# Kernel optimization log

Hardware: AMD Instinct MI355X
Metric: run time of the kernel (lower is better)

## Reference

```python
import jax, jax.numpy as jnp
import numpy as np

# Static problem dims (all graphs equal-sized so adaptive pool = uniform bins)
B = 64          # graphs
N = 2048        # nodes per graph
E = 16          # node_emb_dim
H_OUT, W_OUT = 32, 4   # AdaptiveAvgPool2d output -> pooled_dim = 128
COND = 64       # cond_emb_dim
HID = 512       # mlp_h_dim
BN_EPS = 1e-5


def _lin_init(key, out_d, in_d):
    kw, kb = jax.random.split(key)
    lim = 1.0 / np.sqrt(in_d)
    W = jax.random.uniform(kw, (out_d, in_d), jnp.float32, -lim, lim)
    b = jax.random.uniform(kb, (out_d,), jnp.float32, -lim, lim)
    return W, b


def setup_inputs() -> dict:
    key = jax.random.key(0)
    ks = jax.random.split(key, 6)
    Ntot = B * N
    x = jax.random.normal(ks[0], (Ntot, E), jnp.float32)
    batch = jnp.repeat(jnp.arange(B, dtype=jnp.int32), N)  # sorted segment ids
    cond = jax.random.normal(ks[1], (Ntot, COND), jnp.float32)
    mlp_in = COND + H_OUT * W_OUT  # 192
    W1, b1 = _lin_init(ks[2], HID, mlp_in)
    W2, b2 = _lin_init(ks[3], HID, HID)
    W3, b3 = _lin_init(ks[4], 3, HID)
    g1 = jnp.ones((HID,), jnp.float32); be1 = jnp.zeros((HID,), jnp.float32)
    g2 = jnp.ones((HID,), jnp.float32); be2 = jnp.zeros((HID,), jnp.float32)
    return {"x": x, "batch": batch, "conditioner_z_ref": cond,
            "W1": W1, "b1": b1, "g1": g1, "be1": be1,
            "W2": W2, "b2": b2, "g2": g2, "be2": be2,
            "W3": W3, "b3": b3}


def _bn_gelu(h, g, be):
    # BatchNorm1d in training mode: biased batch stats over the node axis
    m = h.mean(axis=0)
    v = h.var(axis=0)
    h = g * (h - m) * jax.lax.rsqrt(v + BN_EPS) + be
    return jax.nn.gelu(h, approximate=False)


def reference(x, batch, conditioner_z_ref, W1, b1, g1, be1, W2, b2, g2, be2, W3, b3):
    # Per-graph adaptive avg pool: since N % H_OUT == 0 and E % W_OUT == 0,
    # AdaptiveAvgPool2d is exactly mean over uniform (N/H_OUT, E/W_OUT) bins.
    xb = x.reshape(B, H_OUT, N // H_OUT, W_OUT, E // W_OUT)
    batch_pooled = xb.mean(axis=(2, 4)).reshape(B, H_OUT * W_OUT)  # [B, 128]
    pooled_per_node = batch_pooled[batch]                           # gather to [Ntot, 128]
    h = jnp.concatenate([conditioner_z_ref, pooled_per_node], axis=1)  # [Ntot, 192]
    h = _bn_gelu(h @ W1.T + b1, g1, be1)
    h = _bn_gelu(h @ W2.T + b2, g2, be2)
    return h @ W3.T + b3  # [Ntot, 3] predicted coords
```

## Files before the change

### kernel.cpp

```cpp
#include <hip/hip_runtime.h>
#include <hip/hip_bf16.h>
#include <math.h>
#include <stdint.h>

#define B_GRAPHS 64
#define N_NODES  2048
#define E_DIM    16
#define M_TOT    (B_GRAPHS * N_NODES)
#define K_COND   64
#define MLP_IN   192
#define HID      512
#define POOLD    128
#define BN_EPS   1e-5f

typedef __attribute__((ext_vector_type(8))) short bfrag8;
typedef __attribute__((ext_vector_type(4))) float facc4;

__device__ __forceinline__ unsigned short f2b(float f) {
    unsigned int x = __builtin_bit_cast(unsigned int, f);
    unsigned int r = x + 0x7fffu + ((x >> 16) & 1u);
    return (unsigned short)(r >> 16);
}
__device__ __forceinline__ float b2f(unsigned short u) {
    unsigned int x = ((unsigned int)u) << 16;
    return __builtin_bit_cast(float, x);
}

__device__ __forceinline__ float gelu_fast(float y) {
    float x  = y * 0.70710678118654752440f;
    float ax = fabsf(x);
    float t  = __builtin_amdgcn_rcpf(fmaf(0.3275911f, ax, 1.0f));
    float p  = fmaf(1.061405429f, t, -1.453152027f);
    p = fmaf(p, t, 1.421413741f);
    p = fmaf(p, t, -0.284496736f);
    p = fmaf(p, t, 0.254829592f);
    p = p * t;
    float e = __expf(-x * x);
    float erfax = fmaf(-p, e, 1.0f);
    float erfx  = copysignf(erfax, x);
    return 0.5f * y * (1.0f + erfx);
}

__global__ __launch_bounds__(512) void prep_kernel(const float* __restrict__ x,
                                                   const float* __restrict__ W1,
                                                   const float* __restrict__ b1,
                                                   float* __restrict__ gbias) {
    __shared__ float pl[POOLD];
    int g = blockIdx.x, t = threadIdx.x;
    if (t < 128) {
        int h = t >> 2, w = t & 3;
        const float* base = x + (size_t)g * N_NODES * E_DIM + (size_t)h * 64 * E_DIM + w * 4;
        float s = 0.f;
        #pragma unroll 4
        for (int r = 0; r < 64; ++r) {
            float4 v = *reinterpret_cast<const float4*>(base + (size_t)r * E_DIM);
            s += v.x + v.y + v.z + v.w;
        }
        pl[h * 4 + w] = s * (1.0f / 256.0f);
    }
    __syncthreads();
    const float* wr_ = W1 + (size_t)t * MLP_IN + K_COND;
    float s = b1[t];
    #pragma unroll 4
    for (int k = 0; k < POOLD; ++k) s = fmaf(pl[k], wr_[k], s);
    gbias[g * HID + t] = s;
}

__global__ __launch_bounds__(256) void cvt_kernel(const float* __restrict__ s,
                                                  unsigned short* __restrict__ d) {
    size_t i = ((size_t)blockIdx.x * 256 + threadIdx.x) * 8;
    float4 v0 = *reinterpret_cast<const float4*>(s + i);
    float4 v1 = *reinterpret_cast<const float4*>(s + i + 4);
    unsigned short t[8] = {f2b(v0.x), f2b(v0.y), f2b(v0.z), f2b(v0.w),
                           f2b(v1.x), f2b(v1.y), f2b(v1.z), f2b(v1.w)};
    *reinterpret_cast<bfrag8*>(d + i) = *reinterpret_cast<bfrag8*>(t);
}

__device__ __forceinline__ bfrag8 load_f32x8_as_bf16(const float* p) {
    float4 v0 = *reinterpret_cast<const float4*>(p);
    float4 v1 = *reinterpret_cast<const float4*>(p + 4);
    unsigned short t[8] = {f2b(v0.x), f2b(v0.y), f2b(v0.z), f2b(v0.w),
                           f2b(v1.x), f2b(v1.y), f2b(v1.z), f2b(v1.w)};
    return *reinterpret_cast<bfrag8*>(t);
}

__global__ __launch_bounds__(512, 1) void gemm1_kernel(const float* __restrict__ A,
                                                       const float* __restrict__ W,
                                                       const float* __restrict__ gbias,
                                                       float* __restrict__ sums,
                                                       unsigned short* __restrict__ C) {
    __shared__ unsigned short As[128 * 64];
    __shared__ float sArr[HID], qArr[HID];
    const int t = threadIdx.x;
    const int r0 = blockIdx.x * 128;
    const int g = r0 >> 11;
    const int l = t & 63, w = t >> 6;
    const int wr = w >> 2, wc = w & 3;
    const int ln = l & 15, kg = l >> 4;
    sArr[t] = 0.f; qArr[t] = 0.f;

    {
        const int cg = t & 7, rb = t >> 3;
        #pragma unroll
        for (int i = 0; i < 2; ++i) {
            int row = rb + i * 64;
            bfrag8 vv = load_f32x8_as_bf16(A + (size_t)(r0 + row) * K_COND + cg * 8);
            int dg = row * 8 + (cg ^ (row & 7));
            *reinterpret_cast<bfrag8*>(&As[dg * 8]) = vv;
        }
    }
    bfrag8 bf0[8], bf1[8];
    #pragma unroll
    for (int b = 0; b < 8; ++b) {
        int RB = wc * 128 + b * 16 + ln;
        bf0[b] = load_f32x8_as_bf16(W + (size_t)RB * MLP_IN + kg * 8);
        bf1[b] = load_f32x8_as_bf16(W + (size_t)RB * MLP_IN + 32 + kg * 8);
    }
    __syncthreads();

    facc4 acc[4][8];
    const facc4 z = {0.f, 0.f, 0.f, 0.f};
    #pragma unroll
    for (int a = 0; a < 4; ++a)
        #pragma unroll
        for (int b = 0; b < 8; ++b) acc[a][b] = z;

    #pragma unroll
    for (int s = 0; s < 2; ++s) {
        bfrag8 af[4];
        #pragma unroll
        for (int a = 0; a < 4; ++a) {
            int RA = wr * 64 + a * 16 + ln;
            af[a] = *reinterpret_cast<const bfrag8*>(&As[(RA * 8 + ((s * 4 + kg) ^ (RA & 7))) * 8]);
        }
        #pragma unroll
        for (int a = 0; a < 4; ++a)
            #pragma unroll
            for (int b = 0; b < 8; ++b)
                acc[a][b] = __builtin_amdgcn_mfma_f32_16x16x32_bf16(
                    af[a], s == 0 ? bf0[b] : bf1[b], acc[a][b], 0, 0, 0);
    }

    const float* gb = gbias + (size_t)g * HID;
    float gbv[8];
    #pragma unroll
    for (int b = 0; b < 8; ++b) gbv[b] = gb[wc * 128 + b * 16 + ln];
    float cs[8], cq[8];
    #pragma unroll
    for (int b = 0; b < 8; ++b) { cs[b] = 0.f; cq[b] = 0.f; }
    #pragma unroll
    for (int a = 0; a < 4; ++a) {
        #pragma unroll
        for (int i = 0; i < 4; ++i) {
            size_t rbase = (size_t)(r0 + wr * 64 + a * 16 + kg * 4 + i) * HID + wc * 128 + ln;
            #pragma unroll
            for (int b = 0; b < 8; ++b) {
                float v = acc[a][b][i] + gbv[b];
                C[rbase + b * 16] = f2b(v);
                cs[b] += v; cq[b] = fmaf(v, v, cq[b]);
            }
        }
    }
    #pragma unroll
    for (int b = 0; b < 8; ++b) {
        cs[b] += __shfl_xor(cs[b], 16, 64); cq[b] += __shfl_xor(cq[b], 16, 64);
        cs[b] += __shfl_xor(cs[b], 32, 64); cq[b] += __shfl_xor(cq[b], 32, 64);
    }
    if (kg == 0) {
        #pragma unroll
        for (int b = 0; b < 8; ++b) {
            int cl = wc * 128 + b * 16 + ln;
            atomicAdd(&sArr[cl], cs[b]); atomicAdd(&qArr[cl], cq[b]);
        }
    }
    __syncthreads();
    atomicAdd(&sums[t], sArr[t]);
    atomicAdd(&sums[HID + t], qArr[t]);
}

__global__ __launch_bounds__(512, 1) void gemm2_kernel(const unsigned short* __restrict__ A,
                                                       const unsigned short* __restrict__ Bm,
                                                       const float* __restrict__ sums1,
                                                       const float* __restrict__ g1,
                                                       const float* __restrict__ be1,
                                                       const float* __restrict__ bias,
                                                       float* __restrict__ sums,
                                                       unsigned short* __restrict__ C) {
    __shared__ unsigned short As[128 * 512];
    __shared__ float sArr[HID], qArr[HID];
    const int t = threadIdx.x;
    const int r0 = blockIdx.x * 128;
    const int l = t & 63, w = t >> 6;
    const int wr = w >> 2, wc = w & 3;
    const int ln = l & 15, kg = l >> 4;

    sArr[t] = 0.f; qArr[t] = 0.f;

    const int cg = t & 63;
    const int cb = cg * 8;
    float sc[8], sh[8];
    {
        const float inv = 1.0f / (float)M_TOT;
        #pragma unroll
        for (int j = 0; j < 8; ++j) {
            float m_ = sums1[cb + j] * inv;
            float v_ = sums1[HID + cb + j] * inv - m_ * m_;
            float scv = g1[cb + j] * rsqrtf(v_ + BN_EPS);
            sc[j] = scv;
            sh[j] = be1[cb + j] - m_ * scv;
        }
    }

    {
        const int rb = t >> 6;
        bfrag8 v[16];
        #pragma unroll
        for (int i = 0; i < 16; ++i) {
            int row = rb + i * 8;
            v[i] = *reinterpret_cast<const bfrag8*>(&A[(size_t)(r0 + row) * HID + cb]);
        }
        #pragma unroll
        for (int i = 0; i < 16; ++i) {
            int row = rb + i * 8;
            unsigned short tmp[8];
            #pragma unroll
            for (int j = 0; j < 8; ++j) {
                float xv = b2f((unsigned short)v[i][j]);
                tmp[j] = f2b(gelu_fast(fmaf(xv, sc[j], sh[j])));
            }
            int dg = row * 64 + (cg ^ (row & 7));
            *reinterpret_cast<bfrag8*>(&As[dg * 8]) = *reinterpret_cast<bfrag8*>(tmp);
        }
    }
    bfrag8 bfc[8], bfn[8];
    #pragma unroll
    for (int b = 0; b < 8; ++b) {
        int RB = wc * 128 + b * 16 + ln;
        bfc[b] = *reinterpret_cast<const bfrag8*>(&Bm[(size_t)RB * HID + kg * 8]);
    }
    __syncthreads();

    facc4 acc[4][8];
    const facc4 z = {0.f, 0.f, 0.f, 0.f};
    #pragma unroll
    for (int a = 0; a < 4; ++a)
        #pragma unroll
        for (int b = 0; b < 8; ++b) acc[a][b] = z;

    #pragma unroll
    for (int s = 0; s < 16; ++s) {
        if (s < 15) {
            #pragma unroll
            for (int b = 0; b < 8; ++b) {
                int RB = wc * 128 + b * 16 + ln;
                bfn[b] = *reinterpret_cast<const bfrag8*>(
                    &Bm[(size_t)RB * HID + (s + 1) * 32 + kg * 8]);
            }
        }
        bfrag8 af[4];
        #pragma unroll
        for (int a = 0; a < 4; ++a) {
            int RA = wr * 64 + a * 16 + ln;
            af[a] = *reinterpret_cast<const bfrag8*>(
                &As[(RA * 64 + ((s * 4 + kg) ^ (RA & 7))) * 8]);
        }
        #pragma unroll
        for (int a = 0; a < 4; ++a)
            #pragma unroll
            for (int b = 0; b < 8; ++b)
                acc[a][b] = __builtin_amdgcn_mfma_f32_16x16x32_bf16(af[a], bfc[b], acc[a][b], 0, 0, 0);
        #pragma unroll
        for (int b = 0; b < 8; ++b) bfc[b] = bfn[b];
    }

    float bb[8];
    #pragma unroll
    for (int b = 0; b < 8; ++b) bb[b] = bias[wc * 128 + b * 16 + ln];
    float cs[8], cq[8];
    #pragma unroll
    for (int b = 0; b < 8; ++b) { cs[b] = 0.f; cq[b] = 0.f; }
    #pragma unroll
    for (int a = 0; a < 4; ++a) {
        #pragma unroll
        for (int i = 0; i < 4; ++i) {
            size_t rbase = (size_t)(r0 + wr * 64 + a * 16 + kg * 4 + i) * HID + wc * 128 + ln;
            #pragma unroll
            for (int b = 0; b < 8; ++b) {
                float v = acc[a][b][i] + bb[b];
                C[rbase + b * 16] = f2b(v);
                cs[b] += v; cq[b] = fmaf(v, v, cq[b]);
            }
        }
    }
    #pragma unroll
    for (int b = 0; b < 8; ++b) {
        cs[b] += __shfl_xor(cs[b], 16, 64); cq[b] += __shfl_xor(cq[b], 16, 64);
        cs[b] += __shfl_xor(cs[b], 32, 64); cq[b] += __shfl_xor(cq[b], 32, 64);
    }
    if (kg == 0) {
        #pragma unroll
        for (int b = 0; b < 8; ++b) {
            int cl = wc * 128 + b * 16 + ln;
            atomicAdd(&sArr[cl], cs[b]); atomicAdd(&qArr[cl], cq[b]);
        }
    }
    __syncthreads();
    atomicAdd(&sums[t], sArr[t]);
    atomicAdd(&sums[HID + t], qArr[t]);
}

__global__ void finalize_kernel(const float* __restrict__ sums, const float* __restrict__ g,
                                const float* __restrict__ be, float* __restrict__ ss) {
    int n = threadIdx.x;
    float mean = sums[n] * (1.0f / M_TOT);
    float var = sums[HID + n] * (1.0f / M_TOT) - mean * mean;
    float sc = g[n] * rsqrtf(var + BN_EPS);
    ss[n] = sc;
    ss[HID + n] = be[n] - mean * sc;
}

__global__ __launch_bounds__(256) void g3_kernel(const unsigned short* __restrict__ H2,
                                                 const float* __restrict__ ss2,
                                                 const float* __restrict__ W3,
                                                 const float* __restrict__ b3,
                                                 float* __restrict__ out) {
    __shared__ float lss[2 * HID];
    __shared__ float lw3[3 * HID];
    int t = threadIdx.x;
    for (int i = t; i < 2 * HID; i += 256) lss[i] = ss2[i];
    for (int i = t; i < 3 * HID; i += 256) lw3[i] = W3[i];
    __syncthreads();
    int l = t & 63, w = t >> 6;
    int rsub = l >> 3, lk = l & 7;
    int row = blockIdx.x * 32 + w * 8 + rsub;
    const unsigned short* p = H2 + (size_t)row * HID;
    float o0 = 0.f, o1 = 0.f, o2 = 0.f;
    #pragma unroll
    for (int it = 0; it < 8; ++it) {
        int k = it * 64 + lk * 8;
        bfrag8 v = *reinterpret_cast<const bfrag8*>(p + k);
        #pragma unroll
        for (int j = 0; j < 8; ++j) {
            float x = b2f((unsigned short)v[j]);
            float y = fmaf(x, lss[k + j], lss[HID + k + j]);
            y = gelu_fast(y);
            o0 = fmaf(y, lw3[k + j], o0);
            o1 = fmaf(y, lw3[HID + k + j], o1);
            o2 = fmaf(y, lw3[2 * HID + k + j], o2);
        }
    }
    #pragma unroll
    for (int m = 1; m < 8; m <<= 1) {
        o0 += __shfl_xor(o0, m, 64);
        o1 += __shfl_xor(o1, m, 64);
        o2 += __shfl_xor(o2, m, 64);
    }
    if (lk == 0) {
        out[(size_t)row * 3 + 0] = o0 + b3[0];
        out[(size_t)row * 3 + 1] = o1 + b3[1];
        out[(size_t)row * 3 + 2] = o2 + b3[2];
    }
}

extern "C" void kernel_launch(void* const* d_in, const int* in_sizes, int n_in,
                              void* d_out, int out_size, void* d_ws, size_t ws_size,
                              hipStream_t stream) {
    const float* x     = (const float*)d_in[0];
    const float* cond  = (const float*)d_in[2];
    const float* W1    = (const float*)d_in[3];
    const float* b1    = (const float*)d_in[4];
    const float* g1    = (const float*)d_in[5];
    const float* be1   = (const float*)d_in[6];
    const float* W2    = (const float*)d_in[7];
    const float* b2    = (const float*)d_in[8];
    const float* g2    = (const float*)d_in[9];
    const float* be2   = (const float*)d_in[10];
    const float* W3    = (const float*)d_in[11];
    const float* b3    = (const float*)d_in[12];

    const size_t H_BYTES = (size_t)M_TOT * HID * 2;
    if (ws_size < 2 * H_BYTES) return;
    char* ws = (char*)d_ws;
    unsigned short* H1 = (unsigned short*)ws;
    unsigned short* H2 = (unsigned short*)(ws + H_BYTES);

    float* outf   = (float*)d_out;
    float* gbias  = outf;
    float* sums1  = gbias + B_GRAPHS * HID;
    float* sums2  = sums1 + 2 * HID;
    unsigned short* W2bf = (unsigned short*)(sums2 + 2 * HID);
    float* ss2 = (float*)ws;

    hipMemsetAsync(sums1, 0, 2 * 2 * HID * sizeof(float), stream);

    prep_kernel<<<B_GRAPHS, 512, 0, stream>>>(x, W1, b1, gbias);
    cvt_kernel<<<(HID * HID / 8) / 256, 256, 0, stream>>>(W2, W2bf);

    gemm1_kernel<<<dim3(M_TOT / 128, 1), 512, 0, stream>>>(
        cond, W1, gbias, sums1, H1);

    gemm2_kernel<<<dim3(M_TOT / 128, 1), 512, 0, stream>>>(
        H1, W2bf, sums1, g1, be1, b2, sums2, H2);

    finalize_kernel<<<1, HID, 0, stream>>>(sums2, g2, be2, ss2);

    g3_kernel<<<M_TOT / 32, 256, 0, stream>>>(H2, ss2, W3, b3, outf);
}
```

Baseline: 336.1 us.

## Split BN1+GELU into separate pass and pipeline gemm2 with async LDS loads

The BN1+GELU activation moves out of gemm2 into a standalone act_kernel that writes a pre-swizzled bf16 H1a buffer, with a finalize kernel computing the scale and shift first. gemm2 is rewritten as a 256x256-tile GEMM that double-buffers A and B through LDS using global_load_lds and interleaves barriers with s_setprio around the MFMA blocks. W2 is pre-swizzled in cvt_kernel so it matches the new LDS layout. The aim is better data reuse and overlap of loads with MFMA, at the cost of an extra full read and write of the 128 MB activation tensor.

```diff
diff --git a/kernel.cpp b/kernel.cpp
--- a/kernel.cpp
+++ b/kernel.cpp
@@ -40,6 +40,11 @@
     float erfx  = copysignf(erfax, x);
     return 0.5f * y * (1.0f + erfx);
 }
+
+#define GLOAD_LDS16(g, l)                                                        \
+    __builtin_amdgcn_global_load_lds(                                            \
+        (const __attribute__((address_space(1))) unsigned int*)(const void*)(g), \
+        (__attribute__((address_space(3))) unsigned int*)(void*)(l), 16, 0, 0)
 
 __global__ __launch_bounds__(512) void prep_kernel(const float* __restrict__ x,
                                                    const float* __restrict__ W1,
@@ -66,22 +71,32 @@
     gbias[g * HID + t] = s;
 }
 
-__global__ __launch_bounds__(256) void cvt_kernel(const float* __restrict__ s,
-                                                  unsigned short* __restrict__ d) {
-    size_t i = ((size_t)blockIdx.x * 256 + threadIdx.x) * 8;
-    float4 v0 = *reinterpret_cast<const float4*>(s + i);
-    float4 v1 = *reinterpret_cast<const float4*>(s + i + 4);
-    unsigned short t[8] = {f2b(v0.x), f2b(v0.y), f2b(v0.z), f2b(v0.w),
-                           f2b(v1.x), f2b(v1.y), f2b(v1.z), f2b(v1.w)};
-    *reinterpret_cast<bfrag8*>(d + i) = *reinterpret_cast<bfrag8*>(t);
-}
-
 __device__ __forceinline__ bfrag8 load_f32x8_as_bf16(const float* p) {
     float4 v0 = *reinterpret_cast<const float4*>(p);
     float4 v1 = *reinterpret_cast<const float4*>(p + 4);
     unsigned short t[8] = {f2b(v0.x), f2b(v0.y), f2b(v0.z), f2b(v0.w),
                            f2b(v1.x), f2b(v1.y), f2b(v1.z), f2b(v1.w)};
     return *reinterpret_cast<bfrag8*>(t);
+}
+
+__global__ __launch_bounds__(256) void cvt_kernel(const float* __restrict__ W2,
+                                                  unsigned short* __restrict__ W2s) {
+    int gid = blockIdx.x * 256 + threadIdx.x;
+    int n = gid >> 3, ktt = gid & 7;
+    const float* src = W2 + (size_t)n * HID + ktt * 64;
+    unsigned short* dst = W2s + (size_t)n * HID + ktt * 64;
+    int key = (n >> 1) & 3;
+    #pragma unroll
+    for (int h = 0; h < 2; ++h) {
+        #pragma unroll
+        for (int g = 0; g < 4; ++g) {
+            const float* s8 = src + h * 32 + g * 8;
+            unsigned short tmp[8] = {f2b(s8[0]), f2b(s8[1]), f2b(s8[2]), f2b(s8[3]),
+                                     f2b(s8[4]), f2b(s8[5]), f2b(s8[6]), f2b(s8[7])};
+            *reinterpret_cast<bfrag8*>(dst + h * 32 + (g ^ key) * 8) =
+                *reinterpret_cast<bfrag8*>(tmp);
+        }
+    }
 }
 
 __global__ __launch_bounds__(512, 1) void gemm1_kernel(const float* __restrict__ A,
@@ -178,137 +193,6 @@
     atomicAdd(&sums[HID + t], qArr[t]);
 }
 
-__global__ __launch_bounds__(512, 1) void gemm2_kernel(const unsigned short* __restrict__ A,
-                                                       const unsigned short* __restrict__ Bm,
-                                                       const float* __restrict__ sums1,
-                                                       const float* __restrict__ g1,
-                                                       const float* __restrict__ be1,
-                                                       const float* __restrict__ bias,
-                                                       float* __restrict__ sums,
-                                                       unsigned short* __restrict__ C) {
-    __shared__ unsigned short As[128 * 512];
-    __shared__ float sArr[HID], qArr[HID];
-    const int t = threadIdx.x;
-    const int r0 = blockIdx.x * 128;
-    const int l = t & 63, w = t >> 6;
-    const int wr = w >> 2, wc = w & 3;
-    const int ln = l & 15, kg = l >> 4;
-
-    sArr[t] = 0.f; qArr[t] = 0.f;
-
-    const int cg = t & 63;
-    const int cb = cg * 8;
-    float sc[8], sh[8];
-    {
-        const float inv = 1.0f / (float)M_TOT;
-        #pragma unroll
-        for (int j = 0; j < 8; ++j) {
-            float m_ = sums1[cb + j] * inv;
-            float v_ = sums1[HID + cb + j] * inv - m_ * m_;
-            float scv = g1[cb + j] * rsqrtf(v_ + BN_EPS);
-            sc[j] = scv;
-            sh[j] = be1[cb + j] - m_ * scv;
-        }
-    }
-
-    {
-        const int rb = t >> 6;
-        bfrag8 v[16];
-        #pragma unroll
-        for (int i = 0; i < 16; ++i) {
-            int row = rb + i * 8;
-            v[i] = *reinterpret_cast<const bfrag8*>(&A[(size_t)(r0 + row) * HID + cb]);
-        }
-        #pragma unroll
-        for (int i = 0; i < 16; ++i) {
-            int row = rb + i * 8;
-            unsigned short tmp[8];
-            #pragma unroll
-            for (int j = 0; j < 8; ++j) {
-                float xv = b2f((unsigned short)v[i][j]);
-                tmp[j] = f2b(gelu_fast(fmaf(xv, sc[j], sh[j])));
-            }
-            int dg = row * 64 + (cg ^ (row & 7));
-            *reinterpret_cast<bfrag8*>(&As[dg * 8]) = *reinterpret_cast<bfrag8*>(tmp);
-        }
-    }
-    bfrag8 bfc[8], bfn[8];
-    #pragma unroll
-    for (int b = 0; b < 8; ++b) {
-        int RB = wc * 128 + b * 16 + ln;
-        bfc[b] = *reinterpret_cast<const bfrag8*>(&Bm[(size_t)RB * HID + kg * 8]);
-    }
-    __syncthreads();
-
-    facc4 acc[4][8];
-    const facc4 z = {0.f, 0.f, 0.f, 0.f};
-    #pragma unroll
-    for (int a = 0; a < 4; ++a)
-        #pragma unroll
-        for (int b = 0; b < 8; ++b) acc[a][b] = z;
-
-    #pragma unroll
-    for (int s = 0; s < 16; ++s) {
-        if (s < 15) {
-            #pragma unroll
-            for (int b = 0; b < 8; ++b) {
-                int RB = wc * 128 + b * 16 + ln;
-                bfn[b] = *reinterpret_cast<const bfrag8*>(
-                    &Bm[(size_t)RB * HID + (s + 1) * 32 + kg * 8]);
-            }
-        }
-        bfrag8 af[4];
-        #pragma unroll
-        for (int a = 0; a < 4; ++a) {
-            int RA = wr * 64 + a * 16 + ln;
-            af[a] = *reinterpret_cast<const bfrag8*>(
-                &As[(RA * 64 + ((s * 4 + kg) ^ (RA & 7))) * 8]);
-        }
-        #pragma unroll
-        for (int a = 0; a < 4; ++a)
-            #pragma unroll
-            for (int b = 0; b < 8; ++b)
-                acc[a][b] = __builtin_amdgcn_mfma_f32_16x16x32_bf16(af[a], bfc[b], acc[a][b], 0, 0, 0);
-        #pragma unroll
-        for (int b = 0; b < 8; ++b) bfc[b] = bfn[b];
-    }
-
-    float bb[8];
-    #pragma unroll
-    for (int b = 0; b < 8; ++b) bb[b] = bias[wc * 128 + b * 16 + ln];
-    float cs[8], cq[8];
-    #pragma unroll
-    for (int b = 0; b < 8; ++b) { cs[b] = 0.f; cq[b] = 0.f; }
-    #pragma unroll
-    for (int a = 0; a < 4; ++a) {
-        #pragma unroll
-        for (int i = 0; i < 4; ++i) {
-            size_t rbase = (size_t)(r0 + wr * 64 + a * 16 + kg * 4 + i) * HID + wc * 128 + ln;
-            #pragma unroll
-            for (int b = 0; b < 8; ++b) {
-                float v = acc[a][b][i] + bb[b];
-                C[rbase + b * 16] = f2b(v);
-                cs[b] += v; cq[b] = fmaf(v, v, cq[b]);
-            }
-        }
-    }
-    #pragma unroll
-    for (int b = 0; b < 8; ++b) {
-        cs[b] += __shfl_xor(cs[b], 16, 64); cq[b] += __shfl_xor(cq[b], 16, 64);
-        cs[b] += __shfl_xor(cs[b], 32, 64); cq[b] += __shfl_xor(cq[b], 32, 64);
-    }
-    if (kg == 0) {
-        #pragma unroll
-        for (int b = 0; b < 8; ++b) {
-            int cl = wc * 128 + b * 16 + ln;
-            atomicAdd(&sArr[cl], cs[b]); atomicAdd(&qArr[cl], cq[b]);
-        }
-    }
-    __syncthreads();
-    atomicAdd(&sums[t], sArr[t]);
-    atomicAdd(&sums[HID + t], qArr[t]);
-}
-
 __global__ void finalize_kernel(const float* __restrict__ sums, const float* __restrict__ g,
                                 const float* __restrict__ be, float* __restrict__ ss) {
     int n = threadIdx.x;
@@ -317,6 +201,174 @@
     float sc = g[n] * rsqrtf(var + BN_EPS);
     ss[n] = sc;
     ss[HID + n] = be[n] - mean * sc;
+}
+
+__global__ __launch_bounds__(256) void act_kernel(const unsigned short* __restrict__ H1,
+                                                  const float* __restrict__ ss,
+                                                  unsigned short* __restrict__ H1a) {
+    __shared__ float lss[2 * HID];
+    int t = threadIdx.x;
+    #pragma unroll
+    for (int i = t; i < 2 * HID; i += 256) lss[i] = ss[i];
+    __syncthreads();
+    size_t gid = (size_t)blockIdx.x * 256 + t;
+    int R = (int)(gid >> 3);
+    int ktt = (int)(gid & 7);
+    const unsigned short* src = H1 + (size_t)R * HID + ktt * 64;
+    unsigned short* dst = H1a + (size_t)R * HID + ktt * 64;
+    int key = R & 7;
+    #pragma unroll
+    for (int g = 0; g < 8; ++g) {
+        bfrag8 v = *reinterpret_cast<const bfrag8*>(src + g * 8);
+        unsigned short tmp[8];
+        int cb = ktt * 64 + g * 8;
+        #pragma unroll
+        for (int j = 0; j < 8; ++j) {
+            float xv = b2f((unsigned short)v[j]);
+            tmp[j] = f2b(gelu_fast(fmaf(xv, lss[cb + j], lss[HID + cb + j])));
+        }
+        *reinterpret_cast<bfrag8*>(dst + (g ^ key) * 8) = *reinterpret_cast<bfrag8*>(tmp);
+    }
+}
+
+__global__ __launch_bounds__(512) void gemm2_kernel(const unsigned short* __restrict__ A,
+                                                    const unsigned short* __restrict__ Bm,
+                                                    const float* __restrict__ bias,
+                                                    float* __restrict__ sums,
+                                                    unsigned short* __restrict__ C) {
+    __shared__ unsigned short As[2 * 2 * 8192];
+    __shared__ unsigned short Bs[2 * 2 * 8192];
+    __shared__ float sArr[256], qArr[256];
+    const int t = threadIdx.x;
+    const int r0 = blockIdx.x * 256;
+    const int c0 = blockIdx.y * 256;
+    const int l = t & 63, w = t >> 6;
+    const int wr = w >> 2, wc = w & 3;
+    const int ln = l & 15, kg = l >> 4;
+    if (t < 256) { sArr[t] = 0.f; qArr[t] = 0.f; }
+
+    auto issueA = [&](int kt, int nbuf, int h) {
+        #pragma unroll
+        for (int q = 0; q < 2; ++q) {
+            int R = r0 + q * 128 + h * 64 + w * 8 + (l >> 3);
+            const unsigned short* src = A + (size_t)R * HID + kt * 64 + (l & 7) * 8;
+            GLOAD_LDS16(src, &As[(nbuf * 2 + h) * 8192 + (q * 8 + w) * 512]);
+        }
+    };
+    auto issueB = [&](int kt, int nbuf, int kh) {
+        #pragma unroll
+        for (int q = 0; q < 2; ++q) {
+            int nb = (q * 8 + w) * 16 + (l >> 2);
+            const unsigned short* src = Bm + (size_t)(c0 + nb) * HID + kt * 64 + kh * 32 + (l & 3) * 8;
+            GLOAD_LDS16(src, &Bs[(nbuf * 2 + kh) * 8192 + (q * 8 + w) * 512]);
+        }
+    };
+
+    bfrag8 af[4], bf[4];
+    auto dsA = [&](int cbuf, int mh, int kh) {
+        #pragma unroll
+        for (int a = 0; a < 4; ++a) {
+            int lr = wr * 64 + a * 16 + ln;
+            int gcol = kh * 4 + kg;
+            af[a] = *reinterpret_cast<const bfrag8*>(
+                &As[(cbuf * 2 + mh) * 8192 + lr * 64 + ((gcol ^ (lr & 7)) * 8)]);
+        }
+    };
+    auto dsB = [&](int cbuf, int kh) {
+        #pragma unroll
+        for (int b = 0; b < 4; ++b) {
+            int RB = wc * 64 + b * 16 + ln;
+            bf[b] = *reinterpret_cast<const bfrag8*>(
+                &Bs[(cbuf * 2 + kh) * 8192 + RB * 32 + ((kg ^ ((RB >> 1) & 3)) * 8)]);
+        }
+    };
+
+    facc4 acc[8][4];
+    const facc4 z = {0.f, 0.f, 0.f, 0.f};
+    #pragma unroll
+    for (int ai = 0; ai < 8; ++ai)
+        #pragma unroll
+        for (int b = 0; b < 4; ++b) acc[ai][b] = z;
+
+#define MFMA16(MH)                                                                  \
+    do {                                                                            \
+        __builtin_amdgcn_s_setprio(1);                                              \
+        _Pragma("unroll") for (int a = 0; a < 4; ++a)                               \
+            _Pragma("unroll") for (int b = 0; b < 4; ++b)                           \
+                acc[(MH) * 4 + a][b] = __builtin_amdgcn_mfma_f32_16x16x32_bf16(     \
+                    af[a], bf[b], acc[(MH) * 4 + a][b], 0, 0, 0);                   \
+        __builtin_amdgcn_s_setprio(0);                                              \
+    } while (0)
+
+    issueA(0, 0, 0); issueA(0, 0, 1); issueB(0, 0, 0); issueB(0, 0, 1);
+    asm volatile("s_waitcnt vmcnt(0)" ::: "memory");
+    __syncthreads();
+
+    for (int tt = 0; tt < 8; ++tt) {
+        const int c = tt & 1, n = c ^ 1;
+        const bool st = (tt < 7);
+        dsA(c, 0, 0); dsB(c, 0);
+        if (st) issueA(tt + 1, n, 0);
+        __builtin_amdgcn_s_barrier();
+        MFMA16(0);
+        __builtin_amdgcn_s_barrier();
+        dsA(c, 1, 0);
+        if (st) issueA(tt + 1, n, 1);
+        __builtin_amdgcn_s_barrier();
+        MFMA16(1);
+        if (st) asm volatile("s_waitcnt vmcnt(4)" ::: "memory");
+        else    asm volatile("s_waitcnt vmcnt(0)" ::: "memory");
+        __builtin_amdgcn_s_barrier();
+        dsA(c, 0, 1); dsB(c, 1);
+        if (st) issueB(tt + 1, n, 0);
+        __builtin_amdgcn_s_barrier();
+        MFMA16(0);
+        __builtin_amdgcn_s_barrier();
+        dsA(c, 1, 1);
+        if (st) issueB(tt + 1, n, 1);
+        __builtin_amdgcn_s_barrier();
+        MFMA16(1);
+        if (st) asm volatile("s_waitcnt vmcnt(2)" ::: "memory");
+        __builtin_amdgcn_s_barrier();
+    }
+#undef MFMA16
+
+    float bb[4];
+    #pragma unroll
+    for (int b = 0; b < 4; ++b) bb[b] = bias[c0 + wc * 64 + b * 16 + ln];
+    float cs[4] = {0.f, 0.f, 0.f, 0.f}, cq[4] = {0.f, 0.f, 0.f, 0.f};
+    #pragma unroll
+    for (int ai = 0; ai < 8; ++ai) {
+        #pragma unroll
+        for (int i = 0; i < 4; ++i) {
+            int row = r0 + wr * 128 + (ai >> 2) * 64 + (ai & 3) * 16 + kg * 4 + i;
+            size_t rbase = (size_t)row * HID + c0 + wc * 64 + ln;
+            #pragma unroll
+            for (int b = 0; b < 4; ++b) {
+                float v = acc[ai][b][i] + bb[b];
+                C[rbase + b * 16] = f2b(v);
+                cs[b] += v; cq[b] = fmaf(v, v, cq[b]);
+            }
+        }
+    }
+    #pragma unroll
+    for (int b = 0; b < 4; ++b) {
+        cs[b] += __shfl_xor(cs[b], 16, 64); cq[b] += __shfl_xor(cq[b], 16, 64);
+        cs[b] += __shfl_xor(cs[b], 32, 64); cq[b] += __shfl_xor(cq[b], 32, 64);
+    }
+    __syncthreads();
+    if (kg == 0) {
+        #pragma unroll
+        for (int b = 0; b < 4; ++b) {
+            int cl = wc * 64 + b * 16 + ln;
+            atomicAdd(&sArr[cl], cs[b]); atomicAdd(&qArr[cl], cq[b]);
+        }
+    }
+    __syncthreads();
+    if (t < 256) {
+        atomicAdd(&sums[c0 + t], sArr[t]);
+        atomicAdd(&sums[HID + c0 + t], qArr[t]);
+    }
 }
 
 __global__ __launch_bounds__(256) void g3_kernel(const unsigned short* __restrict__ H2,
@@ -381,28 +433,31 @@
     const size_t H_BYTES = (size_t)M_TOT * HID * 2;
     if (ws_size < 2 * H_BYTES) return;
     char* ws = (char*)d_ws;
-    unsigned short* H1 = (unsigned short*)ws;
-    unsigned short* H2 = (unsigned short*)(ws + H_BYTES);
+    unsigned short* H1   = (unsigned short*)ws;
+    unsigned short* H1a  = (unsigned short*)(ws + H_BYTES);
+    unsigned short* H2o  = (unsigned short*)ws;
+    float*          ss2  = (float*)(ws + H_BYTES);
 
     float* outf   = (float*)d_out;
     float* gbias  = outf;
     float* sums1  = gbias + B_GRAPHS * HID;
     float* sums2  = sums1 + 2 * HID;
-    unsigned short* W2bf = (unsigned short*)(sums2 + 2 * HID);
-    float* ss2 = (float*)ws;
+    float* ss1    = sums2 + 2 * HID;
+    unsigned short* W2s = (unsigned short*)(ss1 + 2 * HID);
 
     hipMemsetAsync(sums1, 0, 2 * 2 * HID * sizeof(float), stream);
 
     prep_kernel<<<B_GRAPHS, 512, 0, stream>>>(x, W1, b1, gbias);
-    cvt_kernel<<<(HID * HID / 8) / 256, 256, 0, stream>>>(W2, W2bf);
+    cvt_kernel<<<(HID * 8) / 256, 256, 0, stream>>>(W2, W2s);
 
     gemm1_kernel<<<dim3(M_TOT / 128, 1), 512, 0, stream>>>(
         cond, W1, gbias, sums1, H1);
-
-    gemm2_kernel<<<dim3(M_TOT / 128, 1), 512, 0, stream>>>(
-        H1, W2bf, sums1, g1, be1, b2, sums2, H2);
-
+    finalize_kernel<<<1, HID, 0, stream>>>(sums1, g1, be1, ss1);
+    act_kernel<<<(M_TOT * 8) / 256, 256, 0, stream>>>(H1, ss1, H1a);
+
+    gemm2_kernel<<<dim3(M_TOT / 256, HID / 256), 512, 0, stream>>>(
+        H1a, W2s, b2, sums2, H2o);
     finalize_kernel<<<1, HID, 0, stream>>>(sums2, g2, be2, ss2);
 
-    g3_kernel<<<M_TOT / 32, 256, 0, stream>>>(H2, ss2, W3, b3, outf);
-}
+    g3_kernel<<<M_TOT / 32, 256, 0, stream>>>(H2o, ss2, W3, b3, outf);
+}
```

New measurement: 435.2 us. 29.5% more time.

## Recompute layer-1 GEMM inside layer-2 kernel instead of storing H1

Applied to the files above, without the earlier changes.

The first GEMM now only accumulates BatchNorm statistics and no longer writes the 128MB bf16 H1 activation. The second kernel recomputes cond@W1 (K=64) per tile with MFMA, applies BN+GELU into shared memory in a new swizzled 4-element layout, then runs the W2 GEMM with a 3-deep register prefetch of B fragments. This trades a cheap recomputation of the small-K GEMM for removing an H1 write and read through HBM.

```diff
diff --git a/kernel.cpp b/kernel.cpp
--- a/kernel.cpp
+++ b/kernel.cpp
@@ -14,6 +14,7 @@
 #define BN_EPS   1e-5f
 
 typedef __attribute__((ext_vector_type(8))) short bfrag8;
+typedef __attribute__((ext_vector_type(4))) short bfrag4;
 typedef __attribute__((ext_vector_type(4))) float facc4;
 
 __device__ __forceinline__ unsigned short f2b(float f) {
@@ -84,11 +85,10 @@
     return *reinterpret_cast<bfrag8*>(t);
 }
 
-__global__ __launch_bounds__(512, 1) void gemm1_kernel(const float* __restrict__ A,
-                                                       const float* __restrict__ W,
-                                                       const float* __restrict__ gbias,
-                                                       float* __restrict__ sums,
-                                                       unsigned short* __restrict__ C) {
+__global__ __launch_bounds__(512, 1) void stats1_kernel(const float* __restrict__ A,
+                                                        const float* __restrict__ W,
+                                                        const float* __restrict__ gbias,
+                                                        float* __restrict__ sums) {
     __shared__ unsigned short As[128 * 64];
     __shared__ float sArr[HID], qArr[HID];
     const int t = threadIdx.x;
@@ -152,142 +152,9 @@
     for (int a = 0; a < 4; ++a) {
         #pragma unroll
         for (int i = 0; i < 4; ++i) {
-            size_t rbase = (size_t)(r0 + wr * 64 + a * 16 + kg * 4 + i) * HID + wc * 128 + ln;
             #pragma unroll
             for (int b = 0; b < 8; ++b) {
                 float v = acc[a][b][i] + gbv[b];
-                C[rbase + b * 16] = f2b(v);
-                cs[b] += v; cq[b] = fmaf(v, v, cq[b]);
-            }
-        }
-    }
-    #pragma unroll
-    for (int b = 0; b < 8; ++b) {
-        cs[b] += __shfl_xor(cs[b], 16, 64); cq[b] += __shfl_xor(cq[b], 16, 64);
-        cs[b] += __shfl_xor(cs[b], 32, 64); cq[b] += __shfl_xor(cq[b], 32, 64);
-    }
-    if (kg == 0) {
-        #pragma unroll
-        for (int b = 0; b < 8; ++b) {
-            int cl = wc * 128 + b * 16 + ln;
-            atomicAdd(&sArr[cl], cs[b]); atomicAdd(&qArr[cl], cq[b]);
-        }
-    }
-    __syncthreads();
-    atomicAdd(&sums[t], sArr[t]);
-    atomicAdd(&sums[HID + t], qArr[t]);
-}
-
-__global__ __launch_bounds__(512, 1) void gemm2_kernel(const unsigned short* __restrict__ A,
-                                                       const unsigned short* __restrict__ Bm,
-                                                       const float* __restrict__ sums1,
-                                                       const float* __restrict__ g1,
-                                                       const float* __restrict__ be1,
-                                                       const float* __restrict__ bias,
-                                                       float* __restrict__ sums,
-                                                       unsigned short* __restrict__ C) {
-    __shared__ unsigned short As[128 * 512];
-    __shared__ float sArr[HID], qArr[HID];
-    const int t = threadIdx.x;
-    const int r0 = blockIdx.x * 128;
-    const int l = t & 63, w = t >> 6;
-    const int wr = w >> 2, wc = w & 3;
-    const int ln = l & 15, kg = l >> 4;
-
-    sArr[t] = 0.f; qArr[t] = 0.f;
-
-    const int cg = t & 63;
-    const int cb = cg * 8;
-    float sc[8], sh[8];
-    {
-        const float inv = 1.0f / (float)M_TOT;
-        #pragma unroll
-        for (int j = 0; j < 8; ++j) {
-            float m_ = sums1[cb + j] * inv;
-            float v_ = sums1[HID + cb + j] * inv - m_ * m_;
-            float scv = g1[cb + j] * rsqrtf(v_ + BN_EPS);
-            sc[j] = scv;
-            sh[j] = be1[cb + j] - m_ * scv;
-        }
-    }
-
-    {
-        const int rb = t >> 6;
-        bfrag8 v[16];
-        #pragma unroll
-        for (int i = 0; i < 16; ++i) {
-            int row = rb + i * 8;
-            v[i] = *reinterpret_cast<const bfrag8*>(&A[(size_t)(r0 + row) * HID + cb]);
-        }
-        #pragma unroll
-        for (int i = 0; i < 16; ++i) {
-            int row = rb + i * 8;
-            unsigned short tmp[8];
-            #pragma unroll
-            for (int j = 0; j < 8; ++j) {
-                float xv = b2f((unsigned short)v[i][j]);
-                tmp[j] = f2b(gelu_fast(fmaf(xv, sc[j], sh[j])));
-            }
-            int dg = row * 64 + (cg ^ (row & 7));
-            *reinterpret_cast<bfrag8*>(&As[dg * 8]) = *reinterpret_cast<bfrag8*>(tmp);
-        }
-    }
-    bfrag8 bfc[8], bfn[8];
-    #pragma unroll
-    for (int b = 0; b < 8; ++b) {
-        int RB = wc * 128 + b * 16 + ln;
-        bfc[b] = *reinterpret_cast<const bfrag8*>(&Bm[(size_t)RB * HID + kg * 8]);
-    }
-    __syncthreads();
-
-    facc4 acc[4][8];
-    const facc4 z = {0.f, 0.f, 0.f, 0.f};
-    #pragma unroll
-    for (int a = 0; a < 4; ++a)
-        #pragma unroll
-        for (int b = 0; b < 8; ++b) acc[a][b] = z;
-
-    #pragma unroll
-    for (int s = 0; s < 16; ++s) {
-        if (s < 15) {
-            #pragma unroll
-            for (int b = 0; b < 8; ++b) {
-                int RB = wc * 128 + b * 16 + ln;
-                bfn[b] = *reinterpret_cast<const bfrag8*>(
-                    &Bm[(size_t)RB * HID + (s + 1) * 32 + kg * 8]);
-            }
-        }
-        bfrag8 af[4];
-        #pragma unroll
-        for (int a = 0; a < 4; ++a) {
-            int RA = wr * 64 + a * 16 + ln;
-            af[a] = *reinterpret_cast<const bfrag8*>(
-                &As[(RA * 64 + ((s * 4 + kg) ^ (RA & 7))) * 8]);
-        }
-        #pragma unroll
-        for (int a = 0; a < 4; ++a)
-            #pragma unroll
-            for (int b = 0; b < 8; ++b)
-                acc[a][b] = __builtin_amdgcn_mfma_f32_16x16x32_bf16(af[a], bfc[b], acc[a][b], 0, 0, 0);
-        #pragma unroll
-        for (int b = 0; b < 8; ++b) bfc[b] = bfn[b];
-    }
-
-    float bb[8];
-    #pragma unroll
-    for (int b = 0; b < 8; ++b) bb[b] = bias[wc * 128 + b * 16 + ln];
-    float cs[8], cq[8];
-    #pragma unroll
-    for (int b = 0; b < 8; ++b) { cs[b] = 0.f; cq[b] = 0.f; }
-    #pragma unroll
-    for (int a = 0; a < 4; ++a) {
-        #pragma unroll
-        for (int i = 0; i < 4; ++i) {
-            size_t rbase = (size_t)(r0 + wr * 64 + a * 16 + kg * 4 + i) * HID + wc * 128 + ln;
-            #pragma unroll
-            for (int b = 0; b < 8; ++b) {
-                float v = acc[a][b][i] + bb[b];
-                C[rbase + b * 16] = f2b(v);
                 cs[b] += v; cq[b] = fmaf(v, v, cq[b]);
             }
         }
@@ -317,6 +184,161 @@
     float sc = g[n] * rsqrtf(var + BN_EPS);
     ss[n] = sc;
     ss[HID + n] = be[n] - mean * sc;
+}
+
+__global__ __launch_bounds__(512, 1) void fused2_kernel(const float* __restrict__ cond,
+                                                        const float* __restrict__ W1,
+                                                        const float* __restrict__ gbias,
+                                                        const float* __restrict__ sums1,
+                                                        const float* __restrict__ g1,
+                                                        const float* __restrict__ be1,
+                                                        const unsigned short* __restrict__ W2bf,
+                                                        const float* __restrict__ bias,
+                                                        float* __restrict__ sums,
+                                                        unsigned short* __restrict__ H2) {
+    __shared__ unsigned short As[128 * 512];
+    __shared__ float lss[2 * HID];
+    __shared__ float sArr[HID], qArr[HID];
+    const int t = threadIdx.x;
+    const int r0 = blockIdx.x * 128;
+    const int g = r0 >> 11;
+    const int l = t & 63, w = t >> 6;
+    const int wr = w >> 2, wc = w & 3;
+    const int ln = l & 15, kg = l >> 4;
+
+    {
+        const float inv = 1.0f / (float)M_TOT;
+        float mean = sums1[t] * inv;
+        float var  = sums1[HID + t] * inv - mean * mean;
+        float sc   = g1[t] * rsqrtf(var + BN_EPS);
+        lss[t] = sc;
+        lss[HID + t] = be1[t] - mean * sc;
+    }
+    sArr[t] = 0.f; qArr[t] = 0.f;
+    __syncthreads();
+
+    {
+        facc4 accT[8][4];
+        const facc4 z = {0.f, 0.f, 0.f, 0.f};
+        #pragma unroll
+        for (int b = 0; b < 8; ++b)
+            #pragma unroll
+            for (int a = 0; a < 4; ++a) accT[b][a] = z;
+
+        #pragma unroll
+        for (int ks = 0; ks < 2; ++ks) {
+            bfrag8 afw[8], bfc[4];
+            #pragma unroll
+            for (int b = 0; b < 8; ++b)
+                afw[b] = load_f32x8_as_bf16(
+                    W1 + (size_t)(wc * 128 + b * 16 + ln) * MLP_IN + ks * 32 + kg * 8);
+            #pragma unroll
+            for (int a = 0; a < 4; ++a)
+                bfc[a] = load_f32x8_as_bf16(
+                    cond + (size_t)(r0 + wr * 64 + a * 16 + ln) * K_COND + ks * 32 + kg * 8);
+            #pragma unroll
+            for (int b = 0; b < 8; ++b)
+                #pragma unroll
+                for (int a = 0; a < 4; ++a)
+                    accT[b][a] = __builtin_amdgcn_mfma_f32_16x16x32_bf16(
+                        afw[b], bfc[a], accT[b][a], 0, 0, 0);
+        }
+        #pragma unroll
+        for (int b = 0; b < 8; ++b) {
+            const int n0 = wc * 128 + b * 16 + kg * 4;
+            facc4 sc4 = *reinterpret_cast<const facc4*>(&lss[n0]);
+            facc4 sh4 = *reinterpret_cast<const facc4*>(&lss[HID + n0]);
+            facc4 gb4 = *reinterpret_cast<const facc4*>(&gbias[(size_t)g * HID + n0]);
+            #pragma unroll
+            for (int a = 0; a < 4; ++a) {
+                const int m = wr * 64 + a * 16 + ln;
+                bfrag4 o;
+                #pragma unroll
+                for (int i = 0; i < 4; ++i) {
+                    float h = accT[b][a][i] + gb4[i];
+                    o[i] = (short)f2b(gelu_fast(fmaf(h, sc4[i], sh4[i])));
+                }
+                const int G = (wc * 32 + b * 4 + kg) ^ (m & 15);
+                *reinterpret_cast<bfrag4*>(&As[m * 512 + G * 4]) = o;
+            }
+        }
+    }
+    __syncthreads();
+
+    facc4 acc[4][8];
+    {
+        const facc4 z = {0.f, 0.f, 0.f, 0.f};
+        #pragma unroll
+        for (int a = 0; a < 4; ++a)
+            #pragma unroll
+            for (int b = 0; b < 8; ++b) acc[a][b] = z;
+    }
+    bfrag8 bfv[3][8];
+#define LOADB(KT, SLOT)                                                          \
+    _Pragma("unroll") for (int b = 0; b < 8; ++b)                                \
+        bfv[SLOT][b] = *reinterpret_cast<const bfrag8*>(                         \
+            &W2bf[(size_t)(wc * 128 + b * 16 + ln) * HID + (KT) * 32 + kg * 8]);
+    LOADB(0, 0);
+    LOADB(1, 1);
+    union U8 { bfrag8 v; bfrag4 h[2]; };
+    #pragma unroll
+    for (int kt = 0; kt < 16; ++kt) {
+        const int cs_ = kt % 3, ns_ = (kt + 2) % 3;
+        if (kt < 14) { LOADB(kt + 2, ns_); }
+        bfrag8 af[4];
+        #pragma unroll
+        for (int a = 0; a < 4; ++a) {
+            const int r = wr * 64 + a * 16 + ln;
+            const int g0 = (8 * kt + 2 * kg) ^ (r & 15);
+            const int g1i = (8 * kt + 2 * kg + 1) ^ (r & 15);
+            U8 u;
+            u.h[0] = *reinterpret_cast<const bfrag4*>(&As[r * 512 + g0 * 4]);
+            u.h[1] = *reinterpret_cast<const bfrag4*>(&As[r * 512 + g1i * 4]);
+            af[a] = u.v;
+        }
+        #pragma unroll
+        for (int a = 0; a < 4; ++a)
+            #pragma unroll
+            for (int b = 0; b < 8; ++b)
+                acc[a][b] = __builtin_amdgcn_mfma_f32_16x16x32_bf16(
+                    af[a], bfv[cs_][b], acc[a][b], 0, 0, 0);
+    }
+#undef LOADB
+
+    float bb[8];
+    #pragma unroll
+    for (int b = 0; b < 8; ++b) bb[b] = bias[wc * 128 + b * 16 + ln];
+    float cs[8], cq[8];
+    #pragma unroll
+    for (int b = 0; b < 8; ++b) { cs[b] = 0.f; cq[b] = 0.f; }
+    #pragma unroll
+    for (int a = 0; a < 4; ++a) {
+        #pragma unroll
+        for (int i = 0; i < 4; ++i) {
+            size_t rbase = (size_t)(r0 + wr * 64 + a * 16 + kg * 4 + i) * HID + wc * 128 + ln;
+            #pragma unroll
+            for (int b = 0; b < 8; ++b) {
+                float v = acc[a][b][i] + bb[b];
+                H2[rbase + b * 16] = f2b(v);
+                cs[b] += v; cq[b] = fmaf(v, v, cq[b]);
+            }
+        }
+    }
+    #pragma unroll
+    for (int b = 0; b < 8; ++b) {
+        cs[b] += __shfl_xor(cs[b], 16, 64); cq[b] += __shfl_xor(cq[b], 16, 64);
+        cs[b] += __shfl_xor(cs[b], 32, 64); cq[b] += __shfl_xor(cq[b], 32, 64);
+    }
+    if (kg == 0) {
+        #pragma unroll
+        for (int b = 0; b < 8; ++b) {
+            int cl = wc * 128 + b * 16 + ln;
+            atomicAdd(&sArr[cl], cs[b]); atomicAdd(&qArr[cl], cq[b]);
+        }
+    }
+    __syncthreads();
+    atomicAdd(&sums[t], sArr[t]);
+    atomicAdd(&sums[HID + t], qArr[t]);
 }
 
 __global__ __launch_bounds__(256) void g3_kernel(const unsigned short* __restrict__ H2,
@@ -379,28 +401,26 @@
     const float* b3    = (const float*)d_in[12];
 
     const size_t H_BYTES = (size_t)M_TOT * HID * 2;
-    if (ws_size < 2 * H_BYTES) return;
+    if (ws_size < H_BYTES + 8192) return;
     char* ws = (char*)d_ws;
-    unsigned short* H1 = (unsigned short*)ws;
-    unsigned short* H2 = (unsigned short*)(ws + H_BYTES);
+    unsigned short* H2  = (unsigned short*)ws;
+    float*          ss2 = (float*)(ws + H_BYTES);
 
     float* outf   = (float*)d_out;
     float* gbias  = outf;
     float* sums1  = gbias + B_GRAPHS * HID;
     float* sums2  = sums1 + 2 * HID;
     unsigned short* W2bf = (unsigned short*)(sums2 + 2 * HID);
-    float* ss2 = (float*)ws;
 
     hipMemsetAsync(sums1, 0, 2 * 2 * HID * sizeof(float), stream);
 
     prep_kernel<<<B_GRAPHS, 512, 0, stream>>>(x, W1, b1, gbias);
     cvt_kernel<<<(HID * HID / 8) / 256, 256, 0, stream>>>(W2, W2bf);
 
-    gemm1_kernel<<<dim3(M_TOT / 128, 1), 512, 0, stream>>>(
-        cond, W1, gbias, sums1, H1);
-
-    gemm2_kernel<<<dim3(M_TOT / 128, 1), 512, 0, stream>>>(
-        H1, W2bf, sums1, g1, be1, b2, sums2, H2);
+    stats1_kernel<<<dim3(M_TOT / 128, 1), 512, 0, stream>>>(cond, W1, gbias, sums1);
+
+    fused2_kernel<<<dim3(M_TOT / 128, 1), 512, 0, stream>>>(
+        cond, W1, gbias, sums1, g1, be1, W2bf, b2, sums2, H2);
 
     finalize_kernel<<<1, HID, 0, stream>>>(sums2, g2, be2, ss2);
 
```

Result: slower. 349.0 us (+3.9%).

## Unfuse BN1+GELU into separate pass and rewrite gemm2 with LDS-staged tiles

Applied to the files above, without the earlier changes.

Moves the BatchNorm1+GELU activation out of gemm2 into its own finalize and in-place elementwise pass over H1. gemm2 becomes a conventional 128x256 tiled GEMM with 256 threads, staging A and W2 K-slices through swizzled LDS via global_load_lds, and splits columns across a 2D grid for more blocks and better occupancy. The trade is an extra full read/write of H1 (128 MB of bf16) plus two launches, in return for a leaner GEMM that keeps little in LDS and re-reads A once per column tile.

```diff
diff --git a/kernel.cpp b/kernel.cpp
--- a/kernel.cpp
+++ b/kernel.cpp
@@ -40,6 +40,11 @@
     float erfx  = copysignf(erfax, x);
     return 0.5f * y * (1.0f + erfx);
 }
+
+#define GLOAD_LDS16(g, l)                                                        \
+    __builtin_amdgcn_global_load_lds(                                            \
+        (const __attribute__((address_space(1))) unsigned int*)(const void*)(g), \
+        (__attribute__((address_space(3))) unsigned int*)(void*)(l), 16, 0, 0)
 
 __global__ __launch_bounds__(512) void prep_kernel(const float* __restrict__ x,
                                                    const float* __restrict__ W1,
@@ -178,137 +183,6 @@
     atomicAdd(&sums[HID + t], qArr[t]);
 }
 
-__global__ __launch_bounds__(512, 1) void gemm2_kernel(const unsigned short* __restrict__ A,
-                                                       const unsigned short* __restrict__ Bm,
-                                                       const float* __restrict__ sums1,
-                                                       const float* __restrict__ g1,
-                                                       const float* __restrict__ be1,
-                                                       const float* __restrict__ bias,
-                                                       float* __restrict__ sums,
-                                                       unsigned short* __restrict__ C) {
-    __shared__ unsigned short As[128 * 512];
-    __shared__ float sArr[HID], qArr[HID];
-    const int t = threadIdx.x;
-    const int r0 = blockIdx.x * 128;
-    const int l = t & 63, w = t >> 6;
-    const int wr = w >> 2, wc = w & 3;
-    const int ln = l & 15, kg = l >> 4;
-
-    sArr[t] = 0.f; qArr[t] = 0.f;
-
-    const int cg = t & 63;
-    const int cb = cg * 8;
-    float sc[8], sh[8];
-    {
-        const float inv = 1.0f / (float)M_TOT;
-        #pragma unroll
-        for (int j = 0; j < 8; ++j) {
-            float m_ = sums1[cb + j] * inv;
-            float v_ = sums1[HID + cb + j] * inv - m_ * m_;
-            float scv = g1[cb + j] * rsqrtf(v_ + BN_EPS);
-            sc[j] = scv;
-            sh[j] = be1[cb + j] - m_ * scv;
-        }
-    }
-
-    {
-        const int rb = t >> 6;
-        bfrag8 v[16];
-        #pragma unroll
-        for (int i = 0; i < 16; ++i) {
-            int row = rb + i * 8;
-            v[i] = *reinterpret_cast<const bfrag8*>(&A[(size_t)(r0 + row) * HID + cb]);
-        }
-        #pragma unroll
-        for (int i = 0; i < 16; ++i) {
-            int row = rb + i * 8;
-            unsigned short tmp[8];
-            #pragma unroll
-            for (int j = 0; j < 8; ++j) {
-                float xv = b2f((unsigned short)v[i][j]);
-                tmp[j] = f2b(gelu_fast(fmaf(xv, sc[j], sh[j])));
-            }
-            int dg = row * 64 + (cg ^ (row & 7));
-            *reinterpret_cast<bfrag8*>(&As[dg * 8]) = *reinterpret_cast<bfrag8*>(tmp);
-        }
-    }
-    bfrag8 bfc[8], bfn[8];
-    #pragma unroll
-    for (int b = 0; b < 8; ++b) {
-        int RB = wc * 128 + b * 16 + ln;
-        bfc[b] = *reinterpret_cast<const bfrag8*>(&Bm[(size_t)RB * HID + kg * 8]);
-    }
-    __syncthreads();
-
-    facc4 acc[4][8];
-    const facc4 z = {0.f, 0.f, 0.f, 0.f};
-    #pragma unroll
-    for (int a = 0; a < 4; ++a)
-        #pragma unroll
-        for (int b = 0; b < 8; ++b) acc[a][b] = z;
-
-    #pragma unroll
-    for (int s = 0; s < 16; ++s) {
-        if (s < 15) {
-            #pragma unroll
-            for (int b = 0; b < 8; ++b) {
-                int RB = wc * 128 + b * 16 + ln;
-                bfn[b] = *reinterpret_cast<const bfrag8*>(
-                    &Bm[(size_t)RB * HID + (s + 1) * 32 + kg * 8]);
-            }
-        }
-        bfrag8 af[4];
-        #pragma unroll
-        for (int a = 0; a < 4; ++a) {
-            int RA = wr * 64 + a * 16 + ln;
-            af[a] = *reinterpret_cast<const bfrag8*>(
-                &As[(RA * 64 + ((s * 4 + kg) ^ (RA & 7))) * 8]);
-        }
-        #pragma unroll
-        for (int a = 0; a < 4; ++a)
-            #pragma unroll
-            for (int b = 0; b < 8; ++b)
-                acc[a][b] = __builtin_amdgcn_mfma_f32_16x16x32_bf16(af[a], bfc[b], acc[a][b], 0, 0, 0);
-        #pragma unroll
-        for (int b = 0; b < 8; ++b) bfc[b] = bfn[b];
-    }
-
-    float bb[8];
-    #pragma unroll
-    for (int b = 0; b < 8; ++b) bb[b] = bias[wc * 128 + b * 16 + ln];
-    float cs[8], cq[8];
-    #pragma unroll
-    for (int b = 0; b < 8; ++b) { cs[b] = 0.f; cq[b] = 0.f; }
-    #pragma unroll
-    for (int a = 0; a < 4; ++a) {
-        #pragma unroll
-        for (int i = 0; i < 4; ++i) {
-            size_t rbase = (size_t)(r0 + wr * 64 + a * 16 + kg * 4 + i) * HID + wc * 128 + ln;
-            #pragma unroll
-            for (int b = 0; b < 8; ++b) {
-                float v = acc[a][b][i] + bb[b];
-                C[rbase + b * 16] = f2b(v);
-                cs[b] += v; cq[b] = fmaf(v, v, cq[b]);
-            }
-        }
-    }
-    #pragma unroll
-    for (int b = 0; b < 8; ++b) {
-        cs[b] += __shfl_xor(cs[b], 16, 64); cq[b] += __shfl_xor(cq[b], 16, 64);
-        cs[b] += __shfl_xor(cs[b], 32, 64); cq[b] += __shfl_xor(cq[b], 32, 64);
-    }
-    if (kg == 0) {
-        #pragma unroll
-        for (int b = 0; b < 8; ++b) {
-            int cl = wc * 128 + b * 16 + ln;
-            atomicAdd(&sArr[cl], cs[b]); atomicAdd(&qArr[cl], cq[b]);
-        }
-    }
-    __syncthreads();
-    atomicAdd(&sums[t], sArr[t]);
-    atomicAdd(&sums[HID + t], qArr[t]);
-}
-
 __global__ void finalize_kernel(const float* __restrict__ sums, const float* __restrict__ g,
                                 const float* __restrict__ be, float* __restrict__ ss) {
     int n = threadIdx.x;
@@ -317,6 +191,116 @@
     float sc = g[n] * rsqrtf(var + BN_EPS);
     ss[n] = sc;
     ss[HID + n] = be[n] - mean * sc;
+}
+
+__global__ __launch_bounds__(256) void act_kernel(unsigned short* __restrict__ H,
+                                                  const float* __restrict__ ss) {
+    size_t idx = ((size_t)blockIdx.x * 256 + threadIdx.x) * 8;
+    int col = (int)(idx & (HID - 1));
+    bfrag8 v = *reinterpret_cast<bfrag8*>(&H[idx]);
+    #pragma unroll
+    for (int j = 0; j < 8; ++j) {
+        float x = b2f((unsigned short)v[j]);
+        float y = fmaf(x, ss[col + j], ss[HID + col + j]);
+        y = gelu_fast(y);
+        v[j] = (short)f2b(y);
+    }
+    *reinterpret_cast<bfrag8*>(&H[idx]) = v;
+}
+
+__global__ __launch_bounds__(256) void gemm2_kernel(const unsigned short* __restrict__ A,
+                                                    const unsigned short* __restrict__ Bm,
+                                                    const float* __restrict__ bias,
+                                                    float* __restrict__ sums,
+                                                    unsigned short* __restrict__ C) {
+    __shared__ unsigned short As[128 * 32];
+    __shared__ unsigned short Bs[256 * 32];
+    __shared__ float sArr[256], qArr[256];
+    const int t = threadIdx.x;
+    const int r0 = blockIdx.x * 128, c0 = blockIdx.y * 256;
+    const int l = t & 63, w = t >> 6;
+    const int wr = w >> 1, wc = w & 1;
+    const int ln = l & 15, kg = l >> 4;
+    const int rr = l >> 2, sp = l & 3;
+    const int bss = sp ^ ((rr >> 1) & 3);
+    if (t < 256) { sArr[t] = 0.f; qArr[t] = 0.f; }
+
+    facc4 acc[4][8];
+    const facc4 z = {0.f, 0.f, 0.f, 0.f};
+    #pragma unroll
+    for (int a = 0; a < 4; ++a)
+        #pragma unroll
+        for (int b = 0; b < 8; ++b) acc[a][b] = z;
+
+    for (int kk = 0; kk < HID; kk += 32) {
+        #pragma unroll
+        for (int c = 0; c < 2; ++c) {
+            int chunk = w * 2 + c;
+            const unsigned short* ga = A + (size_t)(r0 + chunk * 16 + rr) * HID + kk + bss * 8;
+            GLOAD_LDS16(ga, &As[chunk * 512]);
+        }
+        #pragma unroll
+        for (int c = 0; c < 4; ++c) {
+            int chunk = w * 4 + c;
+            const unsigned short* gb = Bm + (size_t)(c0 + chunk * 16 + rr) * HID + kk + bss * 8;
+            GLOAD_LDS16(gb, &Bs[chunk * 512]);
+        }
+        __syncthreads();
+        bfrag8 af[4], bf[8];
+        #pragma unroll
+        for (int a = 0; a < 4; ++a) {
+            int RA = wr * 64 + a * 16 + ln;
+            af[a] = *reinterpret_cast<const bfrag8*>(&As[RA * 32 + (kg ^ ((RA >> 1) & 3)) * 8]);
+        }
+        #pragma unroll
+        for (int b = 0; b < 8; ++b) {
+            int RB = wc * 128 + b * 16 + ln;
+            bf[b] = *reinterpret_cast<const bfrag8*>(&Bs[RB * 32 + (kg ^ ((RB >> 1) & 3)) * 8]);
+        }
+        #pragma unroll
+        for (int a = 0; a < 4; ++a)
+            #pragma unroll
+            for (int b = 0; b < 8; ++b)
+                acc[a][b] = __builtin_amdgcn_mfma_f32_16x16x32_bf16(af[a], bf[b], acc[a][b], 0, 0, 0);
+        __syncthreads();
+    }
+
+    float bb[8];
+    #pragma unroll
+    for (int b = 0; b < 8; ++b) bb[b] = bias[c0 + wc * 128 + b * 16 + ln];
+    float cs[8], cq[8];
+    #pragma unroll
+    for (int b = 0; b < 8; ++b) { cs[b] = 0.f; cq[b] = 0.f; }
+    #pragma unroll
+    for (int a = 0; a < 4; ++a) {
+        #pragma unroll
+        for (int i = 0; i < 4; ++i) {
+            size_t rbase = (size_t)(r0 + wr * 64 + a * 16 + kg * 4 + i) * HID + c0 + wc * 128 + ln;
+            #pragma unroll
+            for (int b = 0; b < 8; ++b) {
+                float v = acc[a][b][i] + bb[b];
+                C[rbase + b * 16] = f2b(v);
+                cs[b] += v; cq[b] = fmaf(v, v, cq[b]);
+            }
+        }
+    }
+    #pragma unroll
+    for (int b = 0; b < 8; ++b) {
+        cs[b] += __shfl_xor(cs[b], 16, 64); cq[b] += __shfl_xor(cq[b], 16, 64);
+        cs[b] += __shfl_xor(cs[b], 32, 64); cq[b] += __shfl_xor(cq[b], 32, 64);
+    }
+    if (kg == 0) {
+        #pragma unroll
+        for (int b = 0; b < 8; ++b) {
+            int cl = wc * 128 + b * 16 + ln;
+            atomicAdd(&sArr[cl], cs[b]); atomicAdd(&qArr[cl], cq[b]);
+        }
+    }
+    __syncthreads();
+    if (t < 256) {
+        atomicAdd(&sums[c0 + t], sArr[t]);
+        atomicAdd(&sums[HID + c0 + t], qArr[t]);
+    }
 }
 
 __global__ __launch_bounds__(256) void g3_kernel(const unsigned short* __restrict__ H2,
@@ -388,7 +372,8 @@
     float* gbias  = outf;
     float* sums1  = gbias + B_GRAPHS * HID;
     float* sums2  = sums1 + 2 * HID;
-    unsigned short* W2bf = (unsigned short*)(sums2 + 2 * HID);
+    float* ss1    = sums2 + 2 * HID;
+    unsigned short* W2bf = (unsigned short*)(ss1 + 2 * HID);
     float* ss2 = (float*)ws;
 
     hipMemsetAsync(sums1, 0, 2 * 2 * HID * sizeof(float), stream);
@@ -398,10 +383,11 @@
 
     gemm1_kernel<<<dim3(M_TOT / 128, 1), 512, 0, stream>>>(
         cond, W1, gbias, sums1, H1);
-
-    gemm2_kernel<<<dim3(M_TOT / 128, 1), 512, 0, stream>>>(
-        H1, W2bf, sums1, g1, be1, b2, sums2, H2);
-
+    finalize_kernel<<<1, HID, 0, stream>>>(sums1, g1, be1, ss1);
+    act_kernel<<<(M_TOT * HID / 8) / 256, 256, 0, stream>>>(H1, ss1);
+
+    gemm2_kernel<<<dim3(M_TOT / 128, HID / 256), 256, 0, stream>>>(
+        H1, W2bf, b2, sums2, H2);
     finalize_kernel<<<1, HID, 0, stream>>>(sums2, g2, be2, ss2);
 
     g3_kernel<<<M_TOT / 32, 256, 0, stream>>>(H2, ss2, W3, b3, outf);
```

New measurement: 383.7 us. 14.2% more time.
